# Optimization experiments

Measured on AMD Instinct MI355X. Metric: run time of the kernel, lower is better.

Reference implementation:

```python
import jax, jax.numpy as jnp
import numpy as np

N = 40000      # nodes
E = 320000     # edges (no self loops in input; layer adds them)
F_IN = 256
H1, C1 = 4, 128   # layer 1: att_type 'gat', concat=True
H2, C2 = 8, 6     # layer 2: att_type 'linear', concat=False (mean over heads)
BN_EPS = 1e-5
NEG_SLOPE = 0.2


def setup_inputs() -> dict:
    key = jax.random.key(0)
    k = jax.random.split(key, 12)
    x = jax.random.normal(k[0], (N, F_IN), dtype=jnp.float32)
    row = jax.random.randint(k[1], (E,), 0, N)
    off = jax.random.randint(k[2], (E,), 1, N)
    col = (row + off) % N  # guarantees no self-loops (remove_self_loops is then a no-op)
    edge_index = jnp.stack([row, col])
    s1 = 1.0 / np.sqrt(F_IN)
    s2 = 1.0 / np.sqrt(H1 * C1)
    return dict(
        x=x,
        edge_index=edge_index,
        bn1_gamma=jnp.ones((F_IN,), jnp.float32),
        bn1_beta=jnp.zeros((F_IN,), jnp.float32),
        bn1_mean=jax.random.normal(k[3], (F_IN,), jnp.float32) * 0.1,
        bn1_var=jax.random.uniform(k[4], (F_IN,), jnp.float32, 0.5, 1.5),
        W1=jax.random.normal(k[5], (F_IN, H1 * C1), jnp.float32) * s1,
        att1=jax.random.normal(k[6], (1, H1, 2 * C1), jnp.float32) * 0.1,
        b1=jnp.zeros((H1 * C1,), jnp.float32),
        bn2_gamma=jnp.ones((H1 * C1,), jnp.float32),
        bn2_beta=jnp.zeros((H1 * C1,), jnp.float32),
        bn2_mean=jax.random.normal(k[7], (H1 * C1,), jnp.float32) * 0.1,
        bn2_var=jax.random.uniform(k[8], (H1 * C1,), jnp.float32, 0.5, 1.5),
        W2=jax.random.normal(k[9], (H1 * C1, H2 * C2), jnp.float32) * s2,
        att2=jax.random.normal(k[10], (1, H2, 2 * C2), jnp.float32) * 0.1,
        b2=jnp.zeros((C2,), jnp.float32),
    )


def _bn_eval(x, gamma, beta, mean, var):
    # BatchNorm1d in eval mode (running statistics)
    return (x - mean) * (gamma / jnp.sqrt(var + BN_EPS)) + beta


def _segment_softmax(alpha, seg, num_segments):
    # stable softmax over edges grouped by destination node
    m = jax.ops.segment_max(alpha, seg, num_segments=num_segments)
    ex = jnp.exp(alpha - m[seg])
    den = jax.ops.segment_sum(ex, seg, num_segments=num_segments)
    return ex / (den[seg] + 1e-16)


def _geo_layer(x, row, col, W, att, bias, heads, out_c, att_type, concat):
    n = x.shape[0]
    h = (x @ W).reshape(n, heads, out_c)  # [N,H,C]
    h_j = h[col]                          # gather source features per edge [E,H,C]
    if att_type == 'gat':
        # (cat([x_i,x_j]) * att).sum(-1) == per-node left/right projections gathered
        a_i = (h * att[:, :, :out_c]).sum(-1)[row]   # [E,H]
        a_j = (h_j * att[:, :, out_c:]).sum(-1)      # [E,H]
        alpha = jax.nn.leaky_relu(a_i + a_j, NEG_SLOPE)
    elif att_type == 'linear':
        al = (h_j * att[:, :, :out_c]).sum(-1)
        ar = (h_j * att[:, :, out_c:]).sum(-1)
        alpha = jnp.tanh(al + ar)
    else:
        raise ValueError(att_type)
    alpha = _segment_softmax(alpha, row, n)          # neighbor softmax
    msg = h_j * alpha[:, :, None]                    # [E,H,C]
    out = jax.ops.segment_sum(msg, row, num_segments=n)  # scatter-add ('sum' agg)
    if concat:
        out = out.reshape(n, heads * out_c)
    else:
        out = out.mean(axis=1)
    return out + bias


def reference(x, edge_index, bn1_gamma, bn1_beta, bn1_mean, bn1_var, W1, att1, b1,
              bn2_gamma, bn2_beta, bn2_mean, bn2_var, W2, att2, b2):
    n = x.shape[0]
    loop = jnp.arange(n, dtype=edge_index.dtype)
    row = jnp.concatenate([edge_index[0], loop])  # add self loops (input has none)
    col = jnp.concatenate([edge_index[1], loop])
    # layer 1: dropout (identity in eval) -> BN -> GeoLayer(gat) -> act 'linear' (identity)
    out = _bn_eval(x, bn1_gamma, bn1_beta, bn1_mean, bn1_var)
    out = _geo_layer(out, row, col, W1, att1, b1, H1, C1, 'gat', True)
    # layer 2: BN -> GeoLayer(linear) -> elu
    out = _bn_eval(out, bn2_gamma, bn2_beta, bn2_mean, bn2_var)
    out = jax.nn.elu(_geo_layer(out, row, col, W2, att2, b2, H2, C2, 'linear', False))
    return jax.nn.log_softmax(out, axis=1)
```

## Files before the change

kernel.cpp:

```cpp
#include <hip/hip_runtime.h>
#include <math.h>

#define NN   40000
#define NP   40064
#define EE   320000
#define ET   (EE + NN)
#define FIN  256
#define D1   512
#define NEG  0.2f
#define CAP  64

typedef unsigned short ushort;
typedef __attribute__((ext_vector_type(8))) short   s16x8;
typedef __attribute__((ext_vector_type(4))) float   f32x4;
typedef __attribute__((ext_vector_type(4))) unsigned short u16x4;

#define GL16(g,s) __builtin_amdgcn_global_load_lds((const __attribute__((address_space(1))) unsigned*)(g), (__attribute__((address_space(3))) unsigned*)(s), 16, 0, 0)

__device__ __forceinline__ float lrelu(float x){ return x > 0.f ? x : NEG*x; }
__device__ __forceinline__ float b2f(ushort u){ return __uint_as_float(((unsigned)u) << 16); }
__device__ __forceinline__ ushort f2bf(float f){
  unsigned u = __float_as_uint(f);
  return (ushort)((u + 0x7fffu + ((u >> 16) & 1u)) >> 16);
}
__device__ __forceinline__ float wmaxf(float v){
#pragma unroll
  for (int o = 32; o > 0; o >>= 1) v = fmaxf(v, __shfl_xor(v, o));
  return v;
}
__device__ __forceinline__ float wsumf(float v){
#pragma unroll
  for (int o = 32; o > 0; o >>= 1) v += __shfl_xor(v, o);
  return v;
}

__global__ __launch_bounds__(1024) void zero_prep_kernel(int* __restrict__ cnt,
                            const float* __restrict__ g1, const float* __restrict__ be1,
                            const float* __restrict__ mu1, const float* __restrict__ va1,
                            const float* __restrict__ g2, const float* __restrict__ be2,
                            const float* __restrict__ mu2, const float* __restrict__ va2,
                            const float* __restrict__ b1,
                            float* __restrict__ sc1, float* __restrict__ sh1,
                            float* __restrict__ sc2, float* __restrict__ sh2)
{
  int i = blockIdx.x*1024 + threadIdx.x;
  if (i < NN) cnt[i] = 0;
  if (blockIdx.x == 0){
    int t = threadIdx.x;
    if (t < FIN){ float s = g1[t]*rsqrtf(va1[t]+1e-5f); sc1[t]=s; sh1[t]=be1[t]-mu1[t]*s; }
    if (t < D1){ float s = g2[t]*rsqrtf(va2[t]+1e-5f); sc2[t]=s; sh2[t]=be2[t]+(b1[t]-mu2[t])*s; }
  }
}

__global__ __launch_bounds__(256) void prep_all_kernel(
    const int* __restrict__ rows, const int* __restrict__ cols,
    int* __restrict__ cnt, int* __restrict__ cs,
    const float* __restrict__ X, const float* __restrict__ sc1,
    const float* __restrict__ sh1, ushort* __restrict__ A,
    const float* __restrict__ W1, const float* __restrict__ W2,
    const float* __restrict__ sc2, const float* __restrict__ sh2,
    const float* __restrict__ att1, const float* __restrict__ att2,
    ushort* __restrict__ K1T, float* __restrict__ c2, float* __restrict__ a2s)
{
  int b = blockIdx.x;
  if (b < 1407){
    int e = b*256 + threadIdx.x;
    if (e >= ET) return;
    int r, c;
    if (e < EE){ r = rows[e]; c = cols[e]; } else { r = e - EE; c = r; }
    int slot = atomicAdd(&cnt[r], 1);
    if (slot < CAP) cs[(r << 6) + slot] = c;
    return;
  }
  if (b < 6407){
    int idx = (b-1407)*256 + threadIdx.x;
    int row = idx >> 5, j = (idx & 31) * 8;
    const float* src = X + (size_t)row*FIN + j;
    float4 v0 = *(const float4*)src, v1 = *(const float4*)(src+4);
    float4 s0 = *(const float4*)(sc1+j), s1 = *(const float4*)(sc1+j+4);
    float4 t0 = *(const float4*)(sh1+j), t1 = *(const float4*)(sh1+j+4);
    u16x4 o0, o1v;
    o0[0]=f2bf(v0.x*s0.x+t0.x); o0[1]=f2bf(v0.y*s0.y+t0.y);
    o0[2]=f2bf(v0.z*s0.z+t0.z); o0[3]=f2bf(v0.w*s0.w+t0.w);
    o1v[0]=f2bf(v1.x*s1.x+t1.x); o1v[1]=f2bf(v1.y*s1.y+t1.y);
    o1v[2]=f2bf(v1.z*s1.z+t1.z); o1v[3]=f2bf(v1.w*s1.w+t1.w);
    *(u16x4*)(A + (size_t)row*FIN + j)     = o0;
    *(u16x4*)(A + (size_t)row*FIN + j + 4) = o1v;
    return;
  }
  if (b < 6631){
    __shared__ float wcol[128];
    int t = b - 6407;
    int k = threadIdx.x;
    if (t >= 200){ K1T[(size_t)t*FIN + k] = 0; return; }
    int h;
    if (t < 192){
      h = t & 3; int j = t >> 2;
      if (k < 128){ int kk = h*128 + k; wcol[k] = W2[(size_t)kk*48 + j] * sc2[kk]; }
    } else {
      h = (t - 192) & 3; int off = ((t - 192) >= 4) ? 128 : 0;
      if (k < 128) wcol[k] = att1[h*256 + off + k];
    }
    __syncthreads();
    const float* wr = W1 + (size_t)k*D1 + h*128;
    float acc = 0.f;
#pragma unroll
    for (int kk = 0; kk < 128; kk += 4){
      float4 wv = *(const float4*)(wr + kk);
      float4 cv = *(const float4*)(wcol + kk);
      acc += wv.x*cv.x + wv.y*cv.y + wv.z*cv.z + wv.w*cv.w;
    }
    K1T[(size_t)t*FIN + k] = f2bf(acc);
    return;
  }
  {
    int bb = b - 6631;
    if (bb == 0 && threadIdx.x < 48){
      int h = threadIdx.x/6, c = threadIdx.x%6;
      a2s[threadIdx.x] = att2[h*12 + c] + att2[h*12 + 6 + c];
    }
    int w = bb*4 + (threadIdx.x >> 6);
    int lane = threadIdx.x & 63;
    if (w >= 48) return;
    float acc = 0.f;
    for (int k = lane; k < D1; k += 64) acc += sh2[k] * W2[(size_t)k*48 + w];
    acc = wsumf(acc);
    if (lane == 0) c2[w] = acc;
  }
}

__global__ __launch_bounds__(256) void gemmG_mfma(const ushort* __restrict__ A,
                                                  const ushort* __restrict__ K1T,
                                                  ushort* __restrict__ G,
                                                  float* __restrict__ ai,
                                                  float* __restrict__ aj)
{
  __shared__ ushort As[128*64];
  __shared__ ushort Bs[224*64];
  int row0 = blockIdx.x * 128;
  int tid = threadIdx.x, lane = tid & 63, wave = tid >> 6;
  f32x4 acc[2][13] = {};
  int srow = lane >> 3;
  int scolb = (lane & 7) * 16;
#pragma unroll
  for (int kt = 0; kt < 4; ++kt){
    int k0 = kt*64;
#pragma unroll
    for (int j = 0; j < 4; ++j){
      int c = wave*4 + j;
      int row = c*8 + srow;
      int cb = scolb ^ ((row & 7) << 4);
      GL16((const char*)(A + (size_t)(row0 + row)*FIN + k0) + cb, (char*)As + c*1024);
    }
#pragma unroll
    for (int j = 0; j < 7; ++j){
      int c = wave*7 + j;
      int row = c*8 + srow;
      int cb = scolb ^ ((row & 7) << 4);
      GL16((const char*)(K1T + (size_t)row*FIN + k0) + cb, (char*)Bs + c*1024);
    }
    __syncthreads();
#pragma unroll
    for (int kk = 0; kk < 2; ++kk){
      int kb = kk*64 + (lane >> 4)*16;
      s16x8 a[2];
#pragma unroll
      for (int mi = 0; mi < 2; ++mi){
        int row = wave*32 + mi*16 + (lane & 15);
        a[mi] = *(const s16x8*)((const char*)As + row*128 + (kb ^ ((row & 7) << 4)));
      }
#pragma unroll
      for (int ni = 0; ni < 13; ++ni){
        int row = ni*16 + (lane & 15);
        s16x8 bfrag = *(const s16x8*)((const char*)Bs + row*128 + (kb ^ ((row & 7) << 4)));
#pragma unroll
        for (int mi = 0; mi < 2; ++mi)
          acc[mi][ni] = __builtin_amdgcn_mfma_f32_16x16x32_bf16(a[mi], bfrag, acc[mi][ni], 0, 0, 0);
      }
    }
    __syncthreads();
  }
  int cl = lane & 15;
#pragma unroll
  for (int mi = 0; mi < 2; ++mi){
#pragma unroll
    for (int ni = 0; ni < 12; ++ni){
      int t = ni*16 + cl;
#pragma unroll
      for (int rr = 0; rr < 4; ++rr){
        int row = row0 + wave*32 + mi*16 + (lane >> 4)*4 + rr;
        G[(size_t)row*192 + t] = f2bf(acc[mi][ni][rr]);
      }
    }
    if (cl < 8){
#pragma unroll
      for (int rr = 0; rr < 4; ++rr){
        int row = row0 + wave*32 + mi*16 + (lane >> 4)*4 + rr;
        float v = acc[mi][12][rr];
        if (cl < 4) ai[(size_t)row*4 + cl] = v;
        else        aj[(size_t)row*4 + (cl-4)] = v;
      }
    }
  }
}

__global__ __launch_bounds__(256) void aggA_kernel(const ushort* __restrict__ G,
                                                   const float* __restrict__ ai,
                                                   const float* __restrict__ aj,
                                                   const int* __restrict__ cnt,
                                                   const int* __restrict__ cs,
                                                   const float* __restrict__ c2,
                                                   const float* __restrict__ a2s,
                                                   ushort* __restrict__ PE)
{
  __shared__ float wsh[4][64][4];
  __shared__ int   csh[4][64];
  int lane = threadIdx.x & 63;
  int wave = threadIdx.x >> 6;
  int n = blockIdx.x*4 + wave;
  int deg = cnt[n]; deg = deg > CAP ? CAP : deg;
  float4 an = *(const float4*)(ai + (size_t)n*4);
  bool aclane = lane < 48;
  int lidx = aclane ? lane : 0;
  const char* Gb = (const char*)G + (size_t)lidx*8;
  float acc = 0.f;

  bool act = lane < deg;
  int c = 0;
  float sx=-1e30f, sy=-1e30f, sz=-1e30f, sw=-1e30f;
  if (act){
    c = cs[(n << 6) + lane];
    float4 av = *(const float4*)(aj + (size_t)c*4);
    sx = lrelu(an.x+av.x); sy = lrelu(an.y+av.y);
    sz = lrelu(an.z+av.z); sw = lrelu(an.w+av.w);
  }
  float m0 = wmaxf(sx), m1 = wmaxf(sy), m2 = wmaxf(sz), m3 = wmaxf(sw);
  float e0 = act ? __expf(sx-m0) : 0.f;
  float e1 = act ? __expf(sy-m1) : 0.f;
  float e2 = act ? __expf(sz-m2) : 0.f;
  float e3 = act ? __expf(sw-m3) : 0.f;
  float d0 = wsumf(e0)+1e-16f, d1 = wsumf(e1)+1e-16f;
  float d2 = wsumf(e2)+1e-16f, d3 = wsumf(e3)+1e-16f;
  if (act){
    wsh[wave][lane][0] = e0/d0; wsh[wave][lane][1] = e1/d1;
    wsh[wave][lane][2] = e2/d2; wsh[wave][lane][3] = e3/d3;
    csh[wave][lane] = c*384;
  }
  int e = 0;
  for (; e + 4 <= deg; e += 4){
    int o0 = csh[wave][e],   o1_ = csh[wave][e+1];
    int o2 = csh[wave][e+2], o3  = csh[wave][e+3];
    float4 w0 = *(const float4*)wsh[wave][e];
    float4 w1 = *(const float4*)wsh[wave][e+1];
    float4 w2 = *(const float4*)wsh[wave][e+2];
    float4 w3 = *(const float4*)wsh[wave][e+3];
    u16x4 v0 = *(const u16x4*)(Gb + o0);
    u16x4 v1 = *(const u16x4*)(Gb + o1_);
    u16x4 v2 = *(const u16x4*)(Gb + o2);
    u16x4 v3 = *(const u16x4*)(Gb + o3);
    acc += w0.x*b2f(v0[0]) + w0.y*b2f(v0[1]) + w0.z*b2f(v0[2]) + w0.w*b2f(v0[3]);
    acc += w1.x*b2f(v1[0]) + w1.y*b2f(v1[1]) + w1.z*b2f(v1[2]) + w1.w*b2f(v1[3]);
    acc += w2.x*b2f(v2[0]) + w2.y*b2f(v2[1]) + w2.z*b2f(v2[2]) + w2.w*b2f(v2[3]);
    acc += w3.x*b2f(v3[0]) + w3.y*b2f(v3[1]) + w3.z*b2f(v3[2]) + w3.w*b2f(v3[3]);
  }
  for (; e < deg; ++e){
    int o0 = csh[wave][e];
    float4 w0 = *(const float4*)wsh[wave][e];
    u16x4 v0 = *(const u16x4*)(Gb + o0);
    acc += w0.x*b2f(v0[0]) + w0.y*b2f(v0[1]) + w0.z*b2f(v0[2]) + w0.w*b2f(v0[3]);
  }

  float h = acc + (aclane ? c2[lidx] : 0.f);
  float s = h * (aclane ? a2s[lidx] : 0.f);
  float tot = 0.f;
  int base = (lane/6)*6;
#pragma unroll
  for (int i = 0; i < 6; ++i) tot += __shfl(s, base + i);
  if (aclane){
    float eh = __expf(tanhf(tot));
    ushort* pe = PE + ((size_t)n << 6);
    pe[lane] = f2bf(eh * h);
    if ((lane % 6) == 0) pe[48 + lane/6] = f2bf(eh);
  }
}

__global__ __launch_bounds__(256) void agg2_kernel(const ushort* __restrict__ PE,
                                                   const int* __restrict__ cnt,
                                                   const int* __restrict__ cs,
                                                   const float* __restrict__ bias2,
                                                   float* __restrict__ out)
{
  __shared__ int csh[4][64];
  int lane = threadIdx.x & 63;
  int wave = threadIdx.x >> 6;
  int n = blockIdx.x*4 + wave;
  int deg = cnt[n]; deg = deg > CAP ? CAP : deg;
  int lidx = (lane < 56) ? lane : 0;
  const char* PEb = (const char*)PE + (size_t)lidx*2;
  float acc = 0.f;

  if (lane < deg) csh[wave][lane] = cs[(n << 6) + lane] << 7;
  int e = 0;
  for (; e + 4 <= deg; e += 4){
    int o0 = csh[wave][e],   o1_ = csh[wave][e+1];
    int o2 = csh[wave][e+2], o3  = csh[wave][e+3];
    float v0 = b2f(*(const ushort*)(PEb + o0));
    float v1 = b2f(*(const ushort*)(PEb + o1_));
    float v2 = b2f(*(const ushort*)(PEb + o2));
    float v3 = b2f(*(const ushort*)(PEb + o3));
    acc += (v0 + v1) + (v2 + v3);
  }
  for (; e < deg; ++e)
    acc += b2f(*(const ushort*)(PEb + csh[wave][e]));

  int hh = (lane < 48) ? lane/6 : 0;
  float den = __shfl(acc, 48 + hh);
  float v = acc / den;
  int cc = lane % 6;
  float s = 0.f;
#pragma unroll
  for (int qq = 0; qq < 8; ++qq) s += __shfl(v, cc + 6*qq);
  float val0 = s*(1.f/8.f) + bias2[cc];
  val0 = val0 > 0.f ? val0 : (__expf(val0) - 1.f);
  float val = (lane < 6) ? val0 : -1e30f;
  float mx = val;
#pragma unroll
  for (int o = 1; o < 8; o <<= 1) mx = fmaxf(mx, __shfl_xor(mx, o));
  float ex = (lane < 6) ? __expf(val - mx) : 0.f;
#pragma unroll
  for (int o = 1; o < 8; o <<= 1) ex += __shfl_xor(ex, o);
  if (lane < 6) out[(size_t)n*6 + lane] = val - mx - __logf(ex);
}

extern "C" void kernel_launch(void* const* d_in, const int* in_sizes, int n_in,
                              void* d_out, int out_size, void* d_ws, size_t ws_size,
                              hipStream_t stream)
{
  (void)in_sizes; (void)n_in; (void)out_size; (void)ws_size;
  const float* x   = (const float*)d_in[0];
  const int*   ei  = (const int*)  d_in[1];
  const float* g1  = (const float*)d_in[2];
  const float* be1 = (const float*)d_in[3];
  const float* mu1 = (const float*)d_in[4];
  const float* va1 = (const float*)d_in[5];
  const float* W1  = (const float*)d_in[6];
  const float* at1 = (const float*)d_in[7];
  const float* b1  = (const float*)d_in[8];
  const float* g2  = (const float*)d_in[9];
  const float* be2 = (const float*)d_in[10];
  const float* mu2 = (const float*)d_in[11];
  const float* va2 = (const float*)d_in[12];
  const float* W2  = (const float*)d_in[13];
  const float* at2 = (const float*)d_in[14];
  const float* b2  = (const float*)d_in[15];
  const int* rows = ei;
  const int* cols = ei + EE;
  float* out = (float*)d_out;

  char* p = (char*)d_ws;
  auto carve = [&](size_t bytes)->void*{ void* r = (void*)p; p += (bytes + 255) & ~(size_t)255; return r; };
  ushort* Abf = (ushort*)carve((size_t)NP*FIN*2);
  ushort* K1T = (ushort*)carve((size_t)224*FIN*2);
  ushort* G   = (ushort*)carve((size_t)NP*192*2);
  ushort* PE  = (ushort*)carve((size_t)NN*64*2);
  float* c2   = (float*)carve(48*4);
  float* a2s  = (float*)carve(48*4);
  float* ai   = (float*)carve((size_t)NP*4*4);
  float* aj   = (float*)carve((size_t)NP*4*4);
  float* sc1  = (float*)carve(FIN*4);
  float* sh1  = (float*)carve(FIN*4);
  float* sc2  = (float*)carve(D1*4);
  float* sh2  = (float*)carve(D1*4);
  int* cnt    = (int*)carve((size_t)NN*4);
  int* cs     = (int*)carve((size_t)NN*CAP*4);

  zero_prep_kernel<<<40, 1024, 0, stream>>>(cnt, g1,be1,mu1,va1,g2,be2,mu2,va2,b1,
                                            sc1,sh1,sc2,sh2);
  prep_all_kernel<<<6643, 256, 0, stream>>>(rows, cols, cnt, cs,
                                            x, sc1, sh1, Abf,
                                            W1, W2, sc2, sh2, at1, at2,
                                            K1T, c2, a2s);
  gemmG_mfma<<<313, 256, 0, stream>>>(Abf, K1T, G, ai, aj);
  aggA_kernel<<<NN/4, 256, 0, stream>>>(G, ai, aj, cnt, cs, c2, a2s, PE);
  agg2_kernel<<<NN/4, 256, 0, stream>>>(PE, cnt, cs, b2, out);
}
```

Measured before the change: 110.1 us.

## Fold BN1 into GEMM weights and convert X to bf16 inside the GEMM

BatchNorm-1 scale is folded into the K1T weight matrix and its shift into a per-column bias k0v, which the GEMM epilogue adds. The separate pass that normalized X and wrote a bf16 copy is removed. The GEMM now loads fp32 X directly, converts it to bf16 in registers and stores it into swizzled LDS. This saves a full read+write of the 40000x256 activation matrix, in exchange for synchronous global loads in place of the async global_load_lds path and slightly different rounding, since bf16 is now applied before the affine transform.

```diff
diff --git a/kernel.cpp b/kernel.cpp
--- a/kernel.cpp
+++ b/kernel.cpp
@@ -55,12 +55,12 @@
 __global__ __launch_bounds__(256) void prep_all_kernel(
     const int* __restrict__ rows, const int* __restrict__ cols,
     int* __restrict__ cnt, int* __restrict__ cs,
-    const float* __restrict__ X, const float* __restrict__ sc1,
-    const float* __restrict__ sh1, ushort* __restrict__ A,
     const float* __restrict__ W1, const float* __restrict__ W2,
+    const float* __restrict__ sc1, const float* __restrict__ sh1,
     const float* __restrict__ sc2, const float* __restrict__ sh2,
     const float* __restrict__ att1, const float* __restrict__ att2,
-    ushort* __restrict__ K1T, float* __restrict__ c2, float* __restrict__ a2s)
+    ushort* __restrict__ K1T, float* __restrict__ k0v,
+    float* __restrict__ c2, float* __restrict__ a2s)
 {
   int b = blockIdx.x;
   if (b < 1407){
@@ -72,49 +72,42 @@
     if (slot < CAP) cs[(r << 6) + slot] = c;
     return;
   }
-  if (b < 6407){
-    int idx = (b-1407)*256 + threadIdx.x;
-    int row = idx >> 5, j = (idx & 31) * 8;
-    const float* src = X + (size_t)row*FIN + j;
-    float4 v0 = *(const float4*)src, v1 = *(const float4*)(src+4);
-    float4 s0 = *(const float4*)(sc1+j), s1 = *(const float4*)(sc1+j+4);
-    float4 t0 = *(const float4*)(sh1+j), t1 = *(const float4*)(sh1+j+4);
-    u16x4 o0, o1v;
-    o0[0]=f2bf(v0.x*s0.x+t0.x); o0[1]=f2bf(v0.y*s0.y+t0.y);
-    o0[2]=f2bf(v0.z*s0.z+t0.z); o0[3]=f2bf(v0.w*s0.w+t0.w);
-    o1v[0]=f2bf(v1.x*s1.x+t1.x); o1v[1]=f2bf(v1.y*s1.y+t1.y);
-    o1v[2]=f2bf(v1.z*s1.z+t1.z); o1v[3]=f2bf(v1.w*s1.w+t1.w);
-    *(u16x4*)(A + (size_t)row*FIN + j)     = o0;
-    *(u16x4*)(A + (size_t)row*FIN + j + 4) = o1v;
+  if (b < 1631){
+    __shared__ float wcol[128];
+    __shared__ float red[4];
+    int t = b - 1407;
+    int k = threadIdx.x;
+    float val = 0.f;
+    if (t < 200){
+      int h;
+      if (t < 192){
+        h = t & 3; int j = t >> 2;
+        if (k < 128){ int kk = h*128 + k; wcol[k] = W2[(size_t)kk*48 + j] * sc2[kk]; }
+      } else {
+        h = (t - 192) & 3; int off = ((t - 192) >= 4) ? 128 : 0;
+        if (k < 128) wcol[k] = att1[h*256 + off + k];
+      }
+      __syncthreads();
+      const float* wr = W1 + (size_t)k*D1 + h*128;
+#pragma unroll
+      for (int kk = 0; kk < 128; kk += 4){
+        float4 wv = *(const float4*)(wr + kk);
+        float4 cv = *(const float4*)(wcol + kk);
+        val += wv.x*cv.x + wv.y*cv.y + wv.z*cv.z + wv.w*cv.w;
+      }
+      K1T[(size_t)t*FIN + k] = f2bf(val * sc1[k]);
+      float part = wsumf(sh1[k] * val);
+      if ((k & 63) == 0) red[k >> 6] = part;
+      __syncthreads();
+      if (k == 0) k0v[t] = red[0] + red[1] + red[2] + red[3];
+    } else {
+      K1T[(size_t)t*FIN + k] = 0;
+      if (k == 0) k0v[t] = 0.f;
+    }
     return;
   }
-  if (b < 6631){
-    __shared__ float wcol[128];
-    int t = b - 6407;
-    int k = threadIdx.x;
-    if (t >= 200){ K1T[(size_t)t*FIN + k] = 0; return; }
-    int h;
-    if (t < 192){
-      h = t & 3; int j = t >> 2;
-      if (k < 128){ int kk = h*128 + k; wcol[k] = W2[(size_t)kk*48 + j] * sc2[kk]; }
-    } else {
-      h = (t - 192) & 3; int off = ((t - 192) >= 4) ? 128 : 0;
-      if (k < 128) wcol[k] = att1[h*256 + off + k];
-    }
-    __syncthreads();
-    const float* wr = W1 + (size_t)k*D1 + h*128;
-    float acc = 0.f;
-#pragma unroll
-    for (int kk = 0; kk < 128; kk += 4){
-      float4 wv = *(const float4*)(wr + kk);
-      float4 cv = *(const float4*)(wcol + kk);
-      acc += wv.x*cv.x + wv.y*cv.y + wv.z*cv.z + wv.w*cv.w;
-    }
-    K1T[(size_t)t*FIN + k] = f2bf(acc);
-    return;
-  }
   {
-    int bb = b - 6631;
+    int bb = b - 1631;
     if (bb == 0 && threadIdx.x < 48){
       int h = threadIdx.x/6, c = threadIdx.x%6;
       a2s[threadIdx.x] = att2[h*12 + c] + att2[h*12 + 6 + c];
@@ -129,8 +122,9 @@
   }
 }
 
-__global__ __launch_bounds__(256) void gemmG_mfma(const ushort* __restrict__ A,
+__global__ __launch_bounds__(256) void gemmG_mfma(const float* __restrict__ X,
                                                   const ushort* __restrict__ K1T,
+                                                  const float* __restrict__ k0v,
                                                   ushort* __restrict__ G,
                                                   float* __restrict__ ai,
                                                   float* __restrict__ aj)
@@ -148,9 +142,16 @@
 #pragma unroll
     for (int j = 0; j < 4; ++j){
       int c = wave*4 + j;
-      int row = c*8 + srow;
-      int cb = scolb ^ ((row & 7) << 4);
-      GL16((const char*)(A + (size_t)(row0 + row)*FIN + k0) + cb, (char*)As + c*1024);
+      int rl = c*8 + srow;
+      int rowg = row0 + rl; if (rowg >= NN) rowg = 0;
+      int j0 = ((lane & 7) ^ (rl & 7)) * 8;
+      const float* src = X + (size_t)rowg*FIN + k0 + j0;
+      float4 v0 = *(const float4*)src;
+      float4 v1 = *(const float4*)(src + 4);
+      s16x8 o;
+      o[0]=(short)f2bf(v0.x); o[1]=(short)f2bf(v0.y); o[2]=(short)f2bf(v0.z); o[3]=(short)f2bf(v0.w);
+      o[4]=(short)f2bf(v1.x); o[5]=(short)f2bf(v1.y); o[6]=(short)f2bf(v1.z); o[7]=(short)f2bf(v1.w);
+      *(s16x8*)((char*)As + c*1024 + lane*16) = o;
     }
 #pragma unroll
     for (int j = 0; j < 7; ++j){
@@ -186,17 +187,19 @@
 #pragma unroll
     for (int ni = 0; ni < 12; ++ni){
       int t = ni*16 + cl;
+      float kc = k0v[t];
 #pragma unroll
       for (int rr = 0; rr < 4; ++rr){
         int row = row0 + wave*32 + mi*16 + (lane >> 4)*4 + rr;
-        G[(size_t)row*192 + t] = f2bf(acc[mi][ni][rr]);
+        G[(size_t)row*192 + t] = f2bf(acc[mi][ni][rr] + kc);
       }
     }
     if (cl < 8){
+      float kc = k0v[192 + cl];
 #pragma unroll
       for (int rr = 0; rr < 4; ++rr){
         int row = row0 + wave*32 + mi*16 + (lane >> 4)*4 + rr;
-        float v = acc[mi][12][rr];
+        float v = acc[mi][12][rr] + kc;
         if (cl < 4) ai[(size_t)row*4 + cl] = v;
         else        aj[(size_t)row*4 + (cl-4)] = v;
       }
@@ -359,10 +362,10 @@
 
   char* p = (char*)d_ws;
   auto carve = [&](size_t bytes)->void*{ void* r = (void*)p; p += (bytes + 255) & ~(size_t)255; return r; };
-  ushort* Abf = (ushort*)carve((size_t)NP*FIN*2);
   ushort* K1T = (ushort*)carve((size_t)224*FIN*2);
   ushort* G   = (ushort*)carve((size_t)NP*192*2);
   ushort* PE  = (ushort*)carve((size_t)NN*64*2);
+  float* k0v  = (float*)carve(224*4);
   float* c2   = (float*)carve(48*4);
   float* a2s  = (float*)carve(48*4);
   float* ai   = (float*)carve((size_t)NP*4*4);
@@ -376,11 +379,10 @@
 
   zero_prep_kernel<<<40, 1024, 0, stream>>>(cnt, g1,be1,mu1,va1,g2,be2,mu2,va2,b1,
                                             sc1,sh1,sc2,sh2);
-  prep_all_kernel<<<6643, 256, 0, stream>>>(rows, cols, cnt, cs,
-                                            x, sc1, sh1, Abf,
-                                            W1, W2, sc2, sh2, at1, at2,
-                                            K1T, c2, a2s);
-  gemmG_mfma<<<313, 256, 0, stream>>>(Abf, K1T, G, ai, aj);
+  prep_all_kernel<<<1643, 256, 0, stream>>>(rows, cols, cnt, cs,
+                                            W1, W2, sc1, sh1, sc2, sh2, at1, at2,
+                                            K1T, k0v, c2, a2s);
+  gemmG_mfma<<<313, 256, 0, stream>>>(x, K1T, k0v, G, ai, aj);
   aggA_kernel<<<NN/4, 256, 0, stream>>>(G, ai, aj, cnt, cs, c2, a2s, PE);
   agg2_kernel<<<NN/4, 256, 0, stream>>>(PE, cnt, cs, b2, out);
 }
```

Result: faster. 103.2 us (-6.2%).
